# Kernel optimization log

Hardware: AMD Instinct MI355X
Metric: run time of the kernel (lower is better)

Reference implementation:

```python
import jax, jax.numpy as jnp
import numpy as np

POS_THR = 0.01
EXPANSION = 0.3
HW_RATIO = 2.0


def setup_inputs() -> dict:
    key = jax.random.key(0)
    kp, kj, kv, kg, km = jax.random.split(key, 5)
    B, P, K, H, W = 16, 20, 17, 160, 160
    hm_pred = jax.random.uniform(kp, (B, K, H, W), dtype=jnp.float32)  # some above POS_THR
    gt = jax.random.uniform(kg, (B, K, H, W), dtype=jnp.float32)
    xy = jax.random.uniform(kj, (B, P, K, 2), dtype=jnp.float32) * jnp.array([W, H], jnp.float32)
    v = (jax.random.uniform(kv, (B, P, K, 1)) > 0.3).astype(jnp.float32)
    jointsXYV = jnp.concatenate([xy, v], axis=-1)
    masks = (jax.random.uniform(km, (B, H, W)) > 0.02).astype(jnp.float32)
    return {"hm_pred": hm_pred, "jointsXYV": jointsXYV, "masks": masks, "gt": gt}


def _gen_hm_mask(hm_pred, masks, jointsXYV):
    # hm_pred: [B,K,H,W]; masks: [B,H,W]; jointsXYV: [B,P,K,3]
    B, K, H, W = hm_pred.shape
    f32 = hm_pred.dtype
    vis = (jointsXYV[..., 2] > 0).any(axis=2)          # [B,P] person has any visible joint
    invisible = jointsXYV[..., 2] <= 0                 # [B,P,K]
    xy = jointsXYV[..., :2]                            # [B,P,K,2]
    inf = jnp.asarray(jnp.inf, f32)
    bb_TL = jnp.where(invisible[..., None], inf, xy).min(axis=2)    # [B,P,2]
    bb_BR = jnp.where(invisible[..., None], -inf, xy).max(axis=2)   # [B,P,2]
    bb_WH = jnp.maximum(bb_BR - bb_TL, 1.0)
    bb_CT = 0.5 * (bb_BR + bb_TL)
    bb_WH = jnp.maximum(bb_WH, bb_WH[..., ::-1] / HW_RATIO)
    half = (0.5 + EXPANSION) * bb_WH
    BR = jnp.round(bb_CT + half)
    TL = jnp.round(bb_CT - half)
    gy = jnp.arange(H, dtype=f32)[:, None]             # [H,1]
    gx = jnp.arange(W, dtype=f32)[None, :]             # [1,W]
    minx = TL[..., 0][:, :, None, None]
    miny = TL[..., 1][:, :, None, None]
    maxx = BR[..., 0][:, :, None, None]
    maxy = BR[..., 1][:, :, None, None]
    # True outside the person's expanded bbox  [B,P,H,W]
    outside = (gx < minx) | (gx > maxx) | (gy < miny) | (gy > maxy)
    # per-person per-keypoint mask: 1 keeps pixel; 0 suppresses inside-bbox pixels of
    # invisible keypoints. [B,P,K,H,W]
    paf = outside[:, :, None, :, :] | (~invisible)[:, :, :, None, None]
    # persons with no visible joint were filtered by nonzero() in torch -> neutral (all True)
    paf = paf | (~vis)[:, :, None, None, None]
    allp = paf.all(axis=1)                             # min-reduce over persons  [B,K,H,W]
    hm_masks = jnp.minimum(masks[:, None, :, :], allp.astype(f32))
    hm_masks = jnp.where(hm_pred >= POS_THR, jnp.asarray(1.0, f32), hm_masks)
    return hm_masks


def reference(hm_pred, jointsXYV, masks, gt):
    hm_masks = _gen_hm_mask(hm_pred, masks, jointsXYV)
    loss = (hm_pred - gt) ** 2 * hm_masks
    return loss.mean(axis=(1, 2, 3))  # per-image loss [B]
```

## Files before the change

### kernel.cpp

```cpp
#include <hip/hip_runtime.h>

#define BB 16
#define PP 20
#define KK 17
#define HH 160
#define WW 160
#define PIX (HH * WW)
#define TPB 256
#define VPT 4
#define PIXPERBLK (TPB * VPT)
#define BLKPERB (PIX / PIXPERBLK)
#define NBLK (BB * BLKPERB)
#define POS_THR 0.01f

struct Person {
    float minx, miny, maxx, maxy;
    unsigned int active;
    unsigned int invmask;
};


__global__ void __launch_bounds__(TPB) main_kernel(
        const float* __restrict__ hm, const float* __restrict__ gt,
        const float* __restrict__ masks, const float* __restrict__ joints,
        float* __restrict__ out) {
    __shared__ Person sP[PP];
    int b = blockIdx.x / BLKPERB;
    int blk = blockIdx.x % BLKPERB;

    if (threadIdx.x < PP) {
        const float* j = joints + ((size_t)b * PP + threadIdx.x) * KK * 3;
        float tlx = INFINITY, tly = INFINITY, brx = -INFINITY, bry = -INFINITY;
        unsigned int inv = 0;
        bool anyvis = false;
        #pragma unroll
        for (int k = 0; k < KK; ++k) {
            float x = j[k * 3 + 0];
            float y = j[k * 3 + 1];
            float v = j[k * 3 + 2];
            if (v > 0.0f) {
                anyvis = true;
                tlx = fminf(tlx, x); tly = fminf(tly, y);
                brx = fmaxf(brx, x); bry = fmaxf(bry, y);
            } else {
                inv |= (1u << k);
            }
        }
        Person ps;
        if (!anyvis) {
            ps.active = 0; ps.invmask = 0;
            ps.minx = 0.0f; ps.miny = 0.0f; ps.maxx = -1.0f; ps.maxy = -1.0f;
        } else {
            float w0 = fmaxf(brx - tlx, 1.0f);
            float h0 = fmaxf(bry - tly, 1.0f);
            float cx = 0.5f * (brx + tlx);
            float cy = 0.5f * (bry + tly);
            float w1 = fmaxf(w0, h0 / 2.0f);
            float h1 = fmaxf(h0, w0 / 2.0f);
            float hx = (0.5f + 0.3f) * w1;
            float hy = (0.5f + 0.3f) * h1;
            ps.minx = rintf(cx - hx);
            ps.maxx = rintf(cx + hx);
            ps.miny = rintf(cy - hy);
            ps.maxy = rintf(cy + hy);
            ps.active = 1;
            ps.invmask = inv;
        }
        sP[threadIdx.x] = ps;
    }
    __syncthreads();

    int pix0 = blk * PIXPERBLK + threadIdx.x * VPT;
    int q = pix0 >> 2;
    float gy = (float)(pix0 / WW);
    int x0 = pix0 % WW;

    unsigned int jm0 = 0, jm1 = 0, jm2 = 0, jm3 = 0;
    #pragma unroll
    for (int p = 0; p < PP; ++p) {
        Person ps = sP[p];
        bool iy = (ps.active != 0u) & (gy >= ps.miny) & (gy <= ps.maxy);
        if (iy) {
            float fx0 = (float)x0;
            if ((fx0 >= ps.minx)        & (fx0 <= ps.maxx))        jm0 |= ps.invmask;
            if ((fx0 + 1.0f >= ps.minx) & (fx0 + 1.0f <= ps.maxx)) jm1 |= ps.invmask;
            if ((fx0 + 2.0f >= ps.minx) & (fx0 + 2.0f <= ps.maxx)) jm2 |= ps.invmask;
            if ((fx0 + 3.0f >= ps.minx) & (fx0 + 3.0f <= ps.maxx)) jm3 |= ps.invmask;
        }
    }

    const size_t planeBase = (size_t)b * KK * PIX;
    float4 hbuf[KK], gbuf[KK];
    #pragma unroll
    for (int k = 0; k < KK; ++k)
        hbuf[k] = ((const float4*)(hm + planeBase + (size_t)k * PIX))[q];
    #pragma unroll
    for (int k = 0; k < KK; ++k)
        gbuf[k] = ((const float4*)(gt + planeBase + (size_t)k * PIX))[q];
    float4 mv = ((const float4*)(masks + (size_t)b * PIX))[q];

    float lsum = 0.0f;
    #pragma unroll
    for (int k = 0; k < KK; ++k) {
        float4 h = hbuf[k];
        float4 g = gbuf[k];
        float a0 = ((jm0 >> k) & 1u) ? 0.0f : 1.0f;
        float a1 = ((jm1 >> k) & 1u) ? 0.0f : 1.0f;
        float a2 = ((jm2 >> k) & 1u) ? 0.0f : 1.0f;
        float a3 = ((jm3 >> k) & 1u) ? 0.0f : 1.0f;
        float m0 = (h.x >= POS_THR) ? 1.0f : fminf(mv.x, a0);
        float m1 = (h.y >= POS_THR) ? 1.0f : fminf(mv.y, a1);
        float m2 = (h.z >= POS_THR) ? 1.0f : fminf(mv.z, a2);
        float m3 = (h.w >= POS_THR) ? 1.0f : fminf(mv.w, a3);
        float d0 = h.x - g.x, d1 = h.y - g.y, d2 = h.z - g.z, d3 = h.w - g.w;
        lsum = fmaf(d0 * d0, m0, lsum);
        lsum = fmaf(d1 * d1, m1, lsum);
        lsum = fmaf(d2 * d2, m2, lsum);
        lsum = fmaf(d3 * d3, m3, lsum);
    }

    #pragma unroll
    for (int off = 32; off > 0; off >>= 1) lsum += __shfl_down(lsum, off);
    __shared__ float wsum[4];
    int lane = threadIdx.x & 63;
    int wid = threadIdx.x >> 6;
    if (lane == 0) wsum[wid] = lsum;
    __syncthreads();
    if (threadIdx.x == 0) {
        float s = (wsum[0] + wsum[1]) + (wsum[2] + wsum[3]);
        atomicAdd(&out[b], s / (float)(KK * HH * WW));
    }
}

extern "C" void kernel_launch(void* const* d_in, const int* in_sizes, int n_in,
                              void* d_out, int out_size, void* d_ws, size_t ws_size,
                              hipStream_t stream) {
    const float* hm     = (const float*)d_in[0];
    const float* joints = (const float*)d_in[1];
    const float* masks  = (const float*)d_in[2];
    const float* gt     = (const float*)d_in[3];
    float* out = (float*)d_out;

    main_kernel<<<NBLK, TPB, 0, stream>>>(hm, gt, masks, joints, out);
}
```

Measured before the change: 96.54 us.

## Split keypoint channels across blocks and issue loads before bbox mask computation

Each block now handles a 4-keypoint chunk (the last chunk takes 5) of a pixel segment instead of all 17 keypoints, so the grid grows fourfold (1600 blocks instead of 400) and each thread holds far fewer float4 registers. The global loads for hm, gt and masks are issued before the per-person bbox loop so their latency overlaps with that computation. The cost is that the joint/bbox setup and person loop are repeated four times per pixel, the mask plane is read four times, and there are four times as many atomics.

```diff
diff --git a/kernel.cpp b/kernel.cpp
--- a/kernel.cpp
+++ b/kernel.cpp
@@ -7,10 +7,9 @@
 #define WW 160
 #define PIX (HH * WW)
 #define TPB 256
-#define VPT 4
-#define PIXPERBLK (TPB * VPT)
-#define BLKPERB (PIX / PIXPERBLK)
-#define NBLK (BB * BLKPERB)
+#define SEGS 25
+#define NCH 4
+#define NBLK (BB * SEGS * NCH)
 #define POS_THR 0.01f
 
 struct Person {
@@ -25,8 +24,12 @@
         const float* __restrict__ masks, const float* __restrict__ joints,
         float* __restrict__ out) {
     __shared__ Person sP[PP];
-    int b = blockIdx.x / BLKPERB;
-    int blk = blockIdx.x % BLKPERB;
+    const int b     = blockIdx.x / (SEGS * NCH);
+    const int rem   = blockIdx.x % (SEGS * NCH);
+    const int chunk = rem / SEGS;
+    const int seg   = rem % SEGS;
+    const int ks    = chunk * 4;
+    const bool last = (chunk == 3);
 
     if (threadIdx.x < PP) {
         const float* j = joints + ((size_t)b * PP + threadIdx.x) * KK * 3;
@@ -70,11 +73,25 @@
     }
     __syncthreads();
 
-    int pix0 = blk * PIXPERBLK + threadIdx.x * VPT;
-    int q = pix0 >> 2;
+    const int q = seg * TPB + threadIdx.x;
+    const int pix0 = q * 4;
+    const size_t planeBase = (size_t)b * KK * PIX;
+
+    float4 mv = ((const float4*)(masks + (size_t)b * PIX))[q];
+    float4 hb[5], gb[5];
+    #pragma unroll
+    for (int i = 0; i < 4; ++i)
+        hb[i] = ((const float4*)(hm + planeBase + (size_t)(ks + i) * PIX))[q];
+    #pragma unroll
+    for (int i = 0; i < 4; ++i)
+        gb[i] = ((const float4*)(gt + planeBase + (size_t)(ks + i) * PIX))[q];
+    if (last) {
+        hb[4] = ((const float4*)(hm + planeBase + (size_t)16 * PIX))[q];
+        gb[4] = ((const float4*)(gt + planeBase + (size_t)16 * PIX))[q];
+    }
+
     float gy = (float)(pix0 / WW);
     int x0 = pix0 % WW;
-
     unsigned int jm0 = 0, jm1 = 0, jm2 = 0, jm3 = 0;
     #pragma unroll
     for (int p = 0; p < PP; ++p) {
@@ -89,25 +106,33 @@
         }
     }
 
-    const size_t planeBase = (size_t)b * KK * PIX;
-    float4 hbuf[KK], gbuf[KK];
-    #pragma unroll
-    for (int k = 0; k < KK; ++k)
-        hbuf[k] = ((const float4*)(hm + planeBase + (size_t)k * PIX))[q];
-    #pragma unroll
-    for (int k = 0; k < KK; ++k)
-        gbuf[k] = ((const float4*)(gt + planeBase + (size_t)k * PIX))[q];
-    float4 mv = ((const float4*)(masks + (size_t)b * PIX))[q];
-
     float lsum = 0.0f;
     #pragma unroll
-    for (int k = 0; k < KK; ++k) {
-        float4 h = hbuf[k];
-        float4 g = gbuf[k];
+    for (int i = 0; i < 4; ++i) {
+        int k = ks + i;
+        float4 h = hb[i];
+        float4 g = gb[i];
         float a0 = ((jm0 >> k) & 1u) ? 0.0f : 1.0f;
         float a1 = ((jm1 >> k) & 1u) ? 0.0f : 1.0f;
         float a2 = ((jm2 >> k) & 1u) ? 0.0f : 1.0f;
         float a3 = ((jm3 >> k) & 1u) ? 0.0f : 1.0f;
+        float m0 = (h.x >= POS_THR) ? 1.0f : fminf(mv.x, a0);
+        float m1 = (h.y >= POS_THR) ? 1.0f : fminf(mv.y, a1);
+        float m2 = (h.z >= POS_THR) ? 1.0f : fminf(mv.z, a2);
+        float m3 = (h.w >= POS_THR) ? 1.0f : fminf(mv.w, a3);
+        float d0 = h.x - g.x, d1 = h.y - g.y, d2 = h.z - g.z, d3 = h.w - g.w;
+        lsum = fmaf(d0 * d0, m0, lsum);
+        lsum = fmaf(d1 * d1, m1, lsum);
+        lsum = fmaf(d2 * d2, m2, lsum);
+        lsum = fmaf(d3 * d3, m3, lsum);
+    }
+    if (last) {
+        float4 h = hb[4];
+        float4 g = gb[4];
+        float a0 = ((jm0 >> 16) & 1u) ? 0.0f : 1.0f;
+        float a1 = ((jm1 >> 16) & 1u) ? 0.0f : 1.0f;
+        float a2 = ((jm2 >> 16) & 1u) ? 0.0f : 1.0f;
+        float a3 = ((jm3 >> 16) & 1u) ? 0.0f : 1.0f;
         float m0 = (h.x >= POS_THR) ? 1.0f : fminf(mv.x, a0);
         float m1 = (h.y >= POS_THR) ? 1.0f : fminf(mv.y, a1);
         float m2 = (h.z >= POS_THR) ? 1.0f : fminf(mv.z, a2);
```

New measurement: 113.5 us. 1.18x slower.
